# Kernel optimization log

Hardware: AMD Instinct MI355X
Metric: run time of the kernel (lower is better)

Reference implementation:

```python
import jax, jax.numpy as jnp
import numpy as np

H = 1024          # hidden_size
NH = 16           # num_attention_heads
HD = H // NH      # attention_head_size (= rotary_dim)
I = 4096          # intermediate_size
E = 8             # num_experts
TOPK = 2          # top_k_experts
EPS = 1e-12       # layer_norm_eps
B, S = 2, 2048


def setup_inputs() -> dict:
    key = jax.random.key(0)
    ks = jax.random.split(key, 12)
    sc = 0.02
    return {
        "hidden_states": jax.random.normal(ks[0], (B, S, H), dtype=jnp.float32),
        "Wq": jax.random.normal(ks[1], (H, H), dtype=jnp.float32) * sc,
        "Wk": jax.random.normal(ks[2], (H, H), dtype=jnp.float32) * sc,
        "Wv": jax.random.normal(ks[3], (H, H), dtype=jnp.float32) * sc,
        "Wd": jax.random.normal(ks[4], (H, H), dtype=jnp.float32) * sc,
        "bd": jnp.zeros((H,), dtype=jnp.float32),
        "ln1_g": jnp.ones((H,), dtype=jnp.float32),
        "ln1_b": jnp.zeros((H,), dtype=jnp.float32),
        "Wg": jax.random.normal(ks[5], (H, E), dtype=jnp.float32) * sc,
        "W1": jax.random.normal(ks[6], (E, H, I), dtype=jnp.float32) * sc,
        "W2": jax.random.normal(ks[7], (E, I, H), dtype=jnp.float32) * sc,
        "ln2_g": jnp.ones((H,), dtype=jnp.float32),
        "ln2_b": jnp.zeros((H,), dtype=jnp.float32),
    }


def _layernorm(x, g, b):
    mu = jnp.mean(x, axis=-1, keepdims=True)
    var = jnp.mean(jnp.square(x - mu), axis=-1, keepdims=True)
    return (x - mu) * jax.lax.rsqrt(var + EPS) * g + b


def _rotate_half(x):
    x1, x2 = x[..., : HD // 2], x[..., HD // 2 :]
    return jnp.concatenate((-x2, x1), axis=-1)


def _rope_cos_sin(seq_len, dtype):
    inv_freq = 1.0 / (10000.0 ** (jnp.arange(0, HD, 2, dtype=jnp.float32) / HD))
    t = jnp.arange(seq_len, dtype=jnp.float32)
    freqs = jnp.einsum("i,j->ij", t, inv_freq)          # [S, HD/2]
    emb = jnp.concatenate((freqs, freqs), axis=-1)        # [S, HD]
    return jnp.cos(emb).astype(dtype)[None, None], jnp.sin(emb).astype(dtype)[None, None]


def reference(hidden_states, Wq, Wk, Wv, Wd, bd, ln1_g, ln1_b, Wg, W1, W2, ln2_g, ln2_b):
    b, s, h = hidden_states.shape
    x = hidden_states

    # ---- multi-head attention with RoPE ----
    def heads(z):  # [B,S,H] -> [B,NH,S,HD]
        return z.reshape(b, s, NH, HD).transpose(0, 2, 1, 3)

    q = heads(x @ Wq)
    k = heads(x @ Wk)
    v = heads(x @ Wv)
    cos, sin = _rope_cos_sin(s, q.dtype)
    q = q * cos + _rotate_half(q) * sin
    k = k * cos + _rotate_half(k) * sin

    scores = jnp.einsum("bnqd,bnkd->bnqk", q, k) / jnp.sqrt(jnp.float32(HD)).astype(q.dtype)
    probs = jax.nn.softmax(scores, axis=-1)
    ctx = jnp.einsum("bnqk,bnkd->bnqd", probs, v)
    ctx = ctx.transpose(0, 2, 1, 3).reshape(b, s, h)

    attn_out = ctx @ Wd + bd
    hs = _layernorm(attn_out + x, ln1_g, ln1_b)  # residual + LN

    # ---- MoE ----
    T = b * s
    xt = hs.reshape(T, h)
    router_logits = xt @ Wg                                   # [T, E]
    probs_r = jax.nn.softmax(router_logits.astype(jnp.float32), axis=-1)
    rw, sel = jax.lax.top_k(probs_r, TOPK)                    # [T, K]
    rw = rw / jnp.sum(rw, axis=-1, keepdims=True)

    # aux load-balancing loss
    f_i = jnp.sum(jax.nn.one_hot(sel, E, dtype=jnp.float32), axis=(0, 1)) / T
    P_i = jnp.mean(probs_r, axis=0)
    aux_loss = E * jnp.sum(f_i * P_i)

    # per-token combine weights [T, E] (0 for unrouted experts)
    combine = jnp.zeros((T, E), dtype=jnp.float32)
    combine = combine.at[jnp.arange(T)[:, None], sel].add(rw)
    combine = combine.astype(xt.dtype)

    moe_out = jnp.zeros_like(xt)
    for e in range(E):  # small fixed expert loop
        ye = jax.nn.gelu(xt @ W1[e], approximate=False) @ W2[e]
        moe_out = moe_out + combine[:, e : e + 1] * ye
    moe_out = moe_out.reshape(b, s, h)

    out = _layernorm(hs + moe_out, ln2_g, ln2_b)
    return out, aux_loss
```

## Files before the change

### kernel.cpp

```cpp
#include <hip/hip_runtime.h>
#include <hip/hip_bf16.h>
#include <math.h>

#define H_ 1024
#define NH_ 16
#define HD_ 64
#define I_ 4096
#define E_ 8
#define B_ 2
#define S_ 2048
#define T_ 4096

#define MAXSLOTS 9216
#define MAXTILES 72

typedef __attribute__((ext_vector_type(8))) short short8v;
typedef __attribute__((ext_vector_type(4))) float f32x4;

#define GLOAD16(g, l) __builtin_amdgcn_global_load_lds((const __attribute__((address_space(1))) void*)(g), (__attribute__((address_space(3))) void*)(l), 16, 0, 0)

static __device__ inline unsigned short f2bf(float x) {
    __hip_bfloat16 h = __float2bfloat16(x);
    unsigned short u;
    __builtin_memcpy(&u, &h, 2);
    return u;
}
static __device__ inline float bf2f(unsigned short u) {
    __hip_bfloat16 h;
    __builtin_memcpy(&h, &u, 2);
    return __bfloat162float(h);
}

static __device__ inline float gelu_fast(float x) {
    float z  = x * 0.70710678118654752f;
    float az = fabsf(z);
    float t  = __builtin_amdgcn_rcpf(fmaf(0.3275911f, az, 1.f));
    float p  = fmaf(1.061405429f, t, -1.453152027f);
    p = fmaf(p, t, 1.421413741f);
    p = fmaf(p, t, -0.284496736f);
    p = fmaf(p, t, 0.254829592f);
    p = p * t;
    float e = __expf(-az*az);
    float er = 1.f - p*e;
    er = (z < 0.f) ? -er : er;
    return 0.5f * x * (1.f + er);
}

__global__ __launch_bounds__(256) void prep_inputs(
    const float* __restrict__ x,
    const float* __restrict__ Wq, const float* __restrict__ Wk,
    const float* __restrict__ Wv, const float* __restrict__ Wd,
    __hip_bfloat16* __restrict__ xa_hi, __hip_bfloat16* __restrict__ xa_lo,
    __hip_bfloat16* __restrict__ wqkv_h, __hip_bfloat16* __restrict__ wqkv_l,
    __hip_bfloat16* __restrict__ wd_h, __hip_bfloat16* __restrict__ wd_l)
{
    __shared__ float t[64][65];
    const int bid = blockIdx.x;
    const int tid = threadIdx.x;
    if (bid < 4096) {
        int i = bid * 256 + tid;
        float4 v = ((const float4*)x)[i];
        unsigned short h0 = f2bf(v.x), h1 = f2bf(v.y), h2 = f2bf(v.z), h3 = f2bf(v.w);
        unsigned short l0 = f2bf(v.x - bf2f(h0)), l1 = f2bf(v.y - bf2f(h1));
        unsigned short l2 = f2bf(v.z - bf2f(h2)), l3 = f2bf(v.w - bf2f(h3));
        uint2 ph = make_uint2((unsigned)h0 | ((unsigned)h1 << 16), (unsigned)h2 | ((unsigned)h3 << 16));
        uint2 pl = make_uint2((unsigned)l0 | ((unsigned)l1 << 16), (unsigned)l2 | ((unsigned)l3 << 16));
        *(uint2*)((char*)xa_hi + (size_t)i*8) = ph;
        *(uint2*)((char*)xa_lo + (size_t)i*8) = pl;
        return;
    }
    int tt = bid - 4096;
    int bx = tt & 15, by = (tt >> 4) & 15, z = tt >> 8;
    const float* in = (z==0) ? Wq : (z==1) ? Wk : (z==2) ? Wv : Wd;
    __hip_bfloat16* oh = (z<3) ? (wqkv_h + (size_t)z*1024*1024) : wd_h;
    __hip_bfloat16* ol = (z<3) ? (wqkv_l + (size_t)z*1024*1024) : wd_l;
    int k0 = by*64, n0 = bx*64;
    #pragma unroll
    for (int it=0; it<4; ++it) {
        int lin = it*256 + tid;
        int r = lin >> 4, c4 = (lin & 15) << 2;
        float4 v = *(const float4*)&in[(size_t)(k0+r)*1024 + n0 + c4];
        t[r][c4] = v.x; t[r][c4+1] = v.y; t[r][c4+2] = v.z; t[r][c4+3] = v.w;
    }
    __syncthreads();
    #pragma unroll
    for (int it=0; it<4; ++it) {
        int lin = it*256 + tid;
        int r = lin >> 4, c4 = (lin & 15) << 2;
        float v0 = t[c4][r], v1 = t[c4+1][r], v2 = t[c4+2][r], v3 = t[c4+3][r];
        ushort4 hh, ll;
        hh.x = f2bf(v0); hh.y = f2bf(v1); hh.z = f2bf(v2); hh.w = f2bf(v3);
        ll.x = f2bf(v0 - bf2f(hh.x)); ll.y = f2bf(v1 - bf2f(hh.y));
        ll.z = f2bf(v2 - bf2f(hh.z)); ll.w = f2bf(v3 - bf2f(hh.w));
        size_t o = (size_t)(n0+r)*1024 + k0 + c4;
        *(ushort4*)&oh[o] = hh;
        *(ushort4*)&ol[o] = ll;
    }
}

__global__ __launch_bounds__(256) void transpose_bf16(
    const float* __restrict__ in, __hip_bfloat16* __restrict__ outp, int K, int N)
{
    __shared__ float t[64][65];
    size_t eoff = (size_t)blockIdx.z * (size_t)K * (size_t)N;
    int k0 = blockIdx.y*64, n0 = blockIdx.x*64;
    int tid = threadIdx.x;
    #pragma unroll
    for (int it=0; it<4; ++it) {
        int lin = it*256 + tid;
        int r = lin >> 4, c4 = (lin & 15) << 2;
        float4 v = *(const float4*)&in[eoff + (size_t)(k0+r)*N + n0 + c4];
        t[r][c4] = v.x; t[r][c4+1] = v.y; t[r][c4+2] = v.z; t[r][c4+3] = v.w;
    }
    __syncthreads();
    #pragma unroll
    for (int it=0; it<4; ++it) {
        int lin = it*256 + tid;
        int r = lin >> 4, c4 = (lin & 15) << 2;
        ushort4 o;
        o.x = f2bf(t[c4][r]);   o.y = f2bf(t[c4+1][r]);
        o.z = f2bf(t[c4+2][r]); o.w = f2bf(t[c4+3][r]);
        *(ushort4*)&outp[eoff + (size_t)(n0+r)*K + k0 + c4] = o;
    }
}

__global__ __launch_bounds__(256, 2) void wd_gemm_zero(
    const __hip_bfloat16* __restrict__ Ah, const __hip_bfloat16* __restrict__ Al,
    const __hip_bfloat16* __restrict__ Bh, const __hip_bfloat16* __restrict__ Bl,
    float* __restrict__ C, const float* __restrict__ bias,
    float* __restrict__ moe_out, float* __restrict__ misc16)
{
    const int bid = blockIdx.x;
    const int tid = threadIdx.x;
    if (bid >= 256) {
        int z = bid - 256;
        ((float4*)moe_out)[z*256 + tid] = (float4){0.f,0.f,0.f,0.f};
        if (z == 0 && tid < 16) misc16[tid] = 0.f;
        return;
    }
    const int N = 1024, K = 1024;
    const int w = tid >> 6, lane = tid & 63;
    const int xcd = bid & 7, ix = bid >> 3;
    const int by = xcd*4 + ix / 8;
    const int bx = ix % 8;

    __shared__ __align__(16) char smem[65536];
    const int AH = 0, AL = 16384, BH = 32768, BL = 49152;

    const int laneg = lane >> 3;
    const int k2sw = ((lane & 7) ^ laneg) << 4;
    const int l15 = lane & 15, l4 = lane >> 4;
    const int wr = w >> 1, wc = w & 1;

    f32x4 acc[4][4];
    #pragma unroll
    for (int m=0;m<4;m++)
        #pragma unroll
        for (int n=0;n<4;n++) acc[m][n] = (f32x4){0.f,0.f,0.f,0.f};

    for (int k0 = 0; k0 < K; k0 += 64) {
        __syncthreads();
        #pragma unroll
        for (int qq=0;qq<4;qq++) {
            int arow = by*128 + (w*4+qq)*8 + laneg;
            int brow = bx*128 + (w*4+qq)*8 + laneg;
            size_t aoff = ((size_t)arow*K + k0)*2 + k2sw;
            size_t boff = ((size_t)brow*K + k0)*2 + k2sw;
            GLOAD16((const char*)Ah + aoff, smem + AH + (w*4+qq)*1024);
            GLOAD16((const char*)Al + aoff, smem + AL + (w*4+qq)*1024);
            GLOAD16((const char*)Bh + boff, smem + BH + (w*4+qq)*1024);
            GLOAD16((const char*)Bl + boff, smem + BL + (w*4+qq)*1024);
        }
        __syncthreads();

        short8v ahf[4][2], alf[4][2], bhf[4][2], blf[4][2];
        #pragma unroll
        for (int m=0;m<4;m++) {
            int row = wr*64 + m*16 + l15;
            int rb = row << 7, rsw = (row & 7) << 4;
            #pragma unroll
            for (int s=0;s<2;s++) {
                int off = rb + ((s*64 + (l4<<4)) ^ rsw);
                ahf[m][s] = *(const short8v*)(smem + AH + off);
                alf[m][s] = *(const short8v*)(smem + AL + off);
            }
        }
        #pragma unroll
        for (int n=0;n<4;n++) {
            int row = wc*64 + n*16 + l15;
            int rb = row << 7, rsw = (row & 7) << 4;
            #pragma unroll
            for (int s=0;s<2;s++) {
                int off = rb + ((s*64 + (l4<<4)) ^ rsw);
                bhf[n][s] = *(const short8v*)(smem + BH + off);
                blf[n][s] = *(const short8v*)(smem + BL + off);
            }
        }
        #pragma unroll
        for (int m=0;m<4;m++)
            #pragma unroll
            for (int n=0;n<4;n++)
                #pragma unroll
                for (int s=0;s<2;s++) {
                    acc[m][n] = __builtin_amdgcn_mfma_f32_16x16x32_bf16(ahf[m][s], bhf[n][s], acc[m][n], 0, 0, 0);
                    acc[m][n] = __builtin_amdgcn_mfma_f32_16x16x32_bf16(ahf[m][s], blf[n][s], acc[m][n], 0, 0, 0);
                    acc[m][n] = __builtin_amdgcn_mfma_f32_16x16x32_bf16(alf[m][s], bhf[n][s], acc[m][n], 0, 0, 0);
                }
    }

    #pragma unroll
    for (int m=0;m<4;m++)
        #pragma unroll
        for (int j=0;j<4;j++) {
            int orow = by*128 + wr*64 + m*16 + l4*4 + j;
            #pragma unroll
            for (int n=0;n<4;n++) {
                int ocol = bx*128 + wc*64 + n*16 + l15;
                C[(size_t)orow*N + ocol] = acc[m][n][j] + bias[ocol];
            }
        }
}

__global__ __launch_bounds__(256, 2) void fused_qkv_w12(
    const __hip_bfloat16* __restrict__ Ah, const __hip_bfloat16* __restrict__ Al,
    const __hip_bfloat16* __restrict__ Bh, const __hip_bfloat16* __restrict__ Bl,
    float* __restrict__ C,
    const float* __restrict__ W1, const float* __restrict__ W2,
    __hip_bfloat16* __restrict__ W1t, __hip_bfloat16* __restrict__ W2t)
{
    __shared__ __align__(16) char smem[65536];
    const int tid = threadIdx.x;
    const int bid = blockIdx.x;

    if (bid < 768) {
        const int N = 3072, K = 1024;
        const int w = tid >> 6, lane = tid & 63;
        const int xcd = bid & 7, ix = bid >> 3;
        const int by = xcd*4 + ix / 24;
        const int bx = ix % 24;
        const int AH = 0, AL = 16384, BH = 32768, BL = 49152;
        const int laneg = lane >> 3;
        const int k2sw = ((lane & 7) ^ laneg) << 4;
        const int l15 = lane & 15, l4 = lane >> 4;
        const int wr = w >> 1, wc = w & 1;

        f32x4 acc[4][4];
        #pragma unroll
        for (int m=0;m<4;m++)
            #pragma unroll
            for (int n=0;n<4;n++) acc[m][n] = (f32x4){0.f,0.f,0.f,0.f};

        for (int k0 = 0; k0 < K; k0 += 64) {
            __syncthreads();
            #pragma unroll
            for (int qq=0;qq<4;qq++) {
                int arow = by*128 + (w*4+qq)*8 + laneg;
                int brow = bx*128 + (w*4+qq)*8 + laneg;
                size_t aoff = ((size_t)arow*K + k0)*2 + k2sw;
                size_t boff = ((size_t)brow*K + k0)*2 + k2sw;
                GLOAD16((const char*)Ah + aoff, smem + AH + (w*4+qq)*1024);
                GLOAD16((const char*)Al + aoff, smem + AL + (w*4+qq)*1024);
                GLOAD16((const char*)Bh + boff, smem + BH + (w*4+qq)*1024);
                GLOAD16((const char*)Bl + boff, smem + BL + (w*4+qq)*1024);
            }
            __syncthreads();

            short8v ahf[4][2], alf[4][2], bhf[4][2], blf[4][2];
            #pragma unroll
            for (int m=0;m<4;m++) {
                int row = wr*64 + m*16 + l15;
                int rb = row << 7, rsw = (row & 7) << 4;
                #pragma unroll
                for (int s=0;s<2;s++) {
                    int off = rb + ((s*64 + (l4<<4)) ^ rsw);
                    ahf[m][s] = *(const short8v*)(smem + AH + off);
                    alf[m][s] = *(const short8v*)(smem + AL + off);
                }
            }
            #pragma unroll
            for (int n=0;n<4;n++) {
                int row = wc*64 + n*16 + l15;
                int rb = row << 7, rsw = (row & 7) << 4;
                #pragma unroll
                for (int s=0;s<2;s++) {
                    int off = rb + ((s*64 + (l4<<4)) ^ rsw);
                    bhf[n][s] = *(const short8v*)(smem + BH + off);
                    blf[n][s] = *(const short8v*)(smem + BL + off);
                }
            }
            #pragma unroll
            for (int m=0;m<4;m++)
                #pragma unroll
                for (int n=0;n<4;n++)
                    #pragma unroll
                    for (int s=0;s<2;s++) {
                        acc[m][n] = __builtin_amdgcn_mfma_f32_16x16x32_bf16(ahf[m][s], bhf[n][s], acc[m][n], 0, 0, 0);
                        acc[m][n] = __builtin_amdgcn_mfma_f32_16x16x32_bf16(ahf[m][s], blf[n][s], acc[m][n], 0, 0, 0);
                        acc[m][n] = __builtin_amdgcn_mfma_f32_16x16x32_bf16(alf[m][s], bhf[n][s], acc[m][n], 0, 0, 0);
                    }
        }

        #pragma unroll
        for (int m=0;m<4;m++)
            #pragma unroll
            for (int j=0;j<4;j++) {
                int orow = by*128 + wr*64 + m*16 + l4*4 + j;
                #pragma unroll
                for (int n=0;n<4;n++) {
                    int ocol = bx*128 + wc*64 + n*16 + l15;
                    C[(size_t)orow*N + ocol] = acc[m][n][j];
                }
            }
        return;
    }

    int t = bid - 768;
    const float* src;
    __hip_bfloat16* dst;
    int K, N;
    if (t < 8192) { src = W1; dst = W1t; K = 1024; N = 4096; }
    else          { t -= 8192; src = W2; dst = W2t; K = 4096; N = 1024; }
    const int nb_n = N >> 6;
    int bx = t % nb_n;
    int rest = t / nb_n;
    int by = rest % (K >> 6);
    int bz = rest / (K >> 6);
    size_t eoff = (size_t)bz * (size_t)K * (size_t)N;
    int k0 = by*64, n0 = bx*64;
    float (*tt)[65] = (float(*)[65])smem;
    #pragma unroll
    for (int it=0; it<4; ++it) {
        int lin = it*256 + tid;
        int r = lin >> 4, c4 = (lin & 15) << 2;
        float4 v = *(const float4*)&src[eoff + (size_t)(k0+r)*N + n0 + c4];
        tt[r][c4] = v.x; tt[r][c4+1] = v.y; tt[r][c4+2] = v.z; tt[r][c4+3] = v.w;
    }
    __syncthreads();
    #pragma unroll
    for (int it=0; it<4; ++it) {
        int lin = it*256 + tid;
        int r = lin >> 4, c4 = (lin & 15) << 2;
        ushort4 o;
        o.x = f2bf(tt[c4][r]);   o.y = f2bf(tt[c4+1][r]);
        o.z = f2bf(tt[c4+2][r]); o.w = f2bf(tt[c4+3][r]);
        *(ushort4*)&dst[eoff + (size_t)(n0+r)*K + k0 + c4] = o;
    }
}

template<int MODE, bool PE>
__global__ __launch_bounds__(256) void moe_mfma(
    const __hip_bfloat16* __restrict__ A,
    const __hip_bfloat16* __restrict__ Bt,
    __hip_bfloat16* __restrict__ y1,
    float* __restrict__ moe_out,
    const int* __restrict__ slot_token,
    const float* __restrict__ slot_w,
    const int* __restrict__ tile_expert,
    const int* __restrict__ cnt_ptr,
    const int* __restrict__ base_ptr,
    int N, int K, int nbx)
{
    const int tid = threadIdx.x;
    const int w = tid >> 6, lane = tid & 63;

    int bx, slot0, y1row0;
    const __hip_bfloat16* Bp;
    if (PE) {
        bx = blockIdx.x;
        int tloc = blockIdx.y;
        if ((tloc << 7) >= *cnt_ptr) return;
        slot0 = *base_ptr + (tloc << 7);
        y1row0 = tloc << 7;
        Bp = Bt;
    } else {
        const int wg = blockIdx.x;
        const int xcd = wg & 7, ix = wg >> 3;
        const int byc = (int)(gridDim.x >> 3) / nbx;
        int gt = xcd*byc + ix % byc;
        bx = ix / byc;
        if (gt >= *cnt_ptr) return;
        int e = tile_expert[gt];
        Bp = Bt + (size_t)e * (size_t)K * (size_t)N;
        slot0 = gt << 7;
        y1row0 = gt << 7;
    }

    __shared__ __align__(16) char smem[32768];

    const int laneg = lane >> 3;
    const int k2sw = ((lane & 7) ^ laneg) << 4;

    int tokq[4];
    if (MODE == 2) {
        #pragma unroll
        for (int qq=0;qq<4;qq++) {
            int t0 = slot_token[slot0 + (w*4+qq)*8 + laneg];
            tokq[qq] = t0 < 0 ? 0 : t0;
        }
    }

    f32x4 acc[4][4];
    #pragma unroll
    for (int m=0;m<4;m++)
        #pragma unroll
        for (int n=0;n<4;n++) acc[m][n] = (f32x4){0.f,0.f,0.f,0.f};

    const int l15 = lane & 15;
    const int l4  = lane >> 4;
    const int wr = w >> 1, wc = w & 1;

    for (int k0 = 0; k0 < K; k0 += 64) {
        __syncthreads();
        #pragma unroll
        for (int qq=0;qq<4;qq++) {
            const char* ga;
            if (MODE == 2) {
                ga = (const char*)A + (((size_t)tokq[qq])*K + k0)*2 + k2sw;
            } else {
                int row = y1row0 + (w*4+qq)*8 + laneg;
                ga = (const char*)A + ((size_t)row*K + k0)*2 + k2sw;
            }
            GLOAD16(ga, smem + (w*4+qq)*1024);
        }
        #pragma unroll
        for (int qq=0;qq<4;qq++) {
            int row = bx*128 + (w*4+qq)*8 + laneg;
            const char* gb = (const char*)Bp + ((size_t)row*K + k0)*2 + k2sw;
            GLOAD16(gb, smem + 16384 + (w*4+qq)*1024);
        }
        __syncthreads();

        short8v a_frag[4][2], b_frag[4][2];
        #pragma unroll
        for (int m=0;m<4;m++) {
            int row = wr*64 + m*16 + l15;
            int rb = row << 7;
            #pragma unroll
            for (int s=0;s<2;s++) {
                int off = rb + ((s*64 + (l4<<4)) ^ ((row&7)<<4));
                a_frag[m][s] = *(const short8v*)(smem + off);
            }
        }
        #pragma unroll
        for (int n=0;n<4;n++) {
            int row = wc*64 + n*16 + l15;
            int rb = row << 7;
            #pragma unroll
            for (int s=0;s<2;s++) {
                int off = rb + ((s*64 + (l4<<4)) ^ ((row&7)<<4));
                b_frag[n][s] = *(const short8v*)(smem + 16384 + off);
            }
        }
        #pragma unroll
        for (int m=0;m<4;m++)
            #pragma unroll
            for (int n=0;n<4;n++) {
                acc[m][n] = __builtin_amdgcn_mfma_f32_16x16x32_bf16(a_frag[m][0], b_frag[n][0], acc[m][n], 0, 0, 0);
                acc[m][n] = __builtin_amdgcn_mfma_f32_16x16x32_bf16(a_frag[m][1], b_frag[n][1], acc[m][n], 0, 0, 0);
            }
    }

    if (MODE == 3) {
        #pragma unroll
        for (int m=0;m<4;m++) {
            #pragma unroll
            for (int j=0;j<4;j++) {
                int orow = wr*64 + m*16 + l4*4 + j;
                int slot = slot0 + orow;
                int tok = slot_token[slot];
                if (tok < 0) continue;
                float sw = slot_w[slot];
                #pragma unroll
                for (int n=0;n<4;n++) {
                    int ocol = bx*128 + wc*64 + n*16 + l15;
                    atomicAdd(&moe_out[(size_t)tok*H_ + ocol], sw * acc[m][n][j]);
                }
            }
        }
    } else {
        __syncthreads();
        #pragma unroll
        for (int m=0;m<4;m++)
            #pragma unroll
            for (int j=0;j<4;j++) {
                int orow = wr*64 + m*16 + l4*4 + j;
                #pragma unroll
                for (int n=0;n<4;n++) {
                    int ocol = wc*64 + n*16 + l15;
                    unsigned short g = f2bf(gelu_fast(acc[m][n][j]));
                    *(unsigned short*)(smem + orow*256 + ocol*2) = g;
                }
            }
        __syncthreads();
        #pragma unroll
        for (int s=0;s<8;s++) {
            int row = w*32 + s*4 + l4;
            short8v v = *(const short8v*)(smem + row*256 + l15*16);
            *(short8v*)((char*)y1 + ((size_t)(y1row0 + row)*N + bx*128 + l15*8)*2) = v;
        }
    }
}

__global__ __launch_bounds__(256) void rope_vsplit(
    const float* __restrict__ qkv,
    __hip_bfloat16* __restrict__ qh, __hip_bfloat16* __restrict__ ql,
    __hip_bfloat16* __restrict__ kh, __hip_bfloat16* __restrict__ kl,
    __hip_bfloat16* __restrict__ vth, __hip_bfloat16* __restrict__ vtl)
{
    __shared__ float t[64][65];
    const int bid = blockIdx.x;
    const int tid = threadIdx.x;
    if (bid < 8192) {
        int idx = bid * 256 + tid;
        int i = idx & 31;
        int n = (idx >> 5) & (NH_-1);
        int tk = idx >> 9;
        int b = tk >> 11;
        int pos = tk & (S_ - 1);
        float inv = exp2f((float)i * (-13.287712379549449f / 32.f));
        float ang = (float)pos * inv;
        float c = cosf(ang), s = sinf(ang);
        size_t base = (size_t)tk*3072 + (size_t)n*64;
        size_t obase = ((size_t)(b*NH_ + n)*S_ + pos)*64;

        float q1 = qkv[base+i], q2 = qkv[base+i+32];
        float qo1 = (q1*c - q2*s)*0.125f;
        float qo2 = (q2*c + q1*s)*0.125f;
        unsigned short h1 = f2bf(qo1), h2 = f2bf(qo2);
        qh[obase+i]    = *(__hip_bfloat16*)&h1;
        qh[obase+i+32] = *(__hip_bfloat16*)&h2;
        unsigned short lo1 = f2bf(qo1 - bf2f(h1)), lo2 = f2bf(qo2 - bf2f(h2));
        ql[obase+i]    = *(__hip_bfloat16*)&lo1;
        ql[obase+i+32] = *(__hip_bfloat16*)&lo2;

        float k1 = qkv[base+1024+i], k2 = qkv[base+1024+i+32];
        float ko1 = k1*c - k2*s;
        float ko2 = k2*c + k1*s;
        unsigned short kh1 = f2bf(ko1), kh2 = f2bf(ko2);
        kh[obase+i]    = *(__hip_bfloat16*)&kh1;
        kh[obase+i+32] = *(__hip_bfloat16*)&kh2;
        unsigned short kl1 = f2bf(ko1 - bf2f(kh1)), kl2 = f2bf(ko2 - bf2f(kh2));
        kl[obase+i]    = *(__hip_bfloat16*)&kl1;
        kl[obase+i+32] = *(__hip_bfloat16*)&kl2;
        return;
    }
    int tt = bid - 8192;
    const int s0 = (tt & 31)*64;
    const int hn = (tt >> 5) & 15;
    const int b  = tt >> 9;
    #pragma unroll
    for (int it=0; it<4; ++it) {
        int lin = it*256 + tid;
        int r = lin >> 4, c4 = (lin & 15) << 2;
        float4 vv = *(const float4*)&qkv[(size_t)(b*S_ + s0 + r)*3072 + 2048 + hn*64 + c4];
        t[r][c4] = vv.x; t[r][c4+1] = vv.y; t[r][c4+2] = vv.z; t[r][c4+3] = vv.w;
    }
    __syncthreads();
    size_t obase = (size_t)(b*NH_ + hn)*64*S_;
    #pragma unroll
    for (int it=0; it<4; ++it) {
        int lin = it*256 + tid;
        int d = lin >> 4, c4 = (lin & 15) << 2;
        float v0 = t[c4][d], v1 = t[c4+1][d], v2 = t[c4+2][d], v3 = t[c4+3][d];
        ushort4 hh, ll;
        hh.x = f2bf(v0); hh.y = f2bf(v1); hh.z = f2bf(v2); hh.w = f2bf(v3);
        ll.x = f2bf(v0 - bf2f(hh.x)); ll.y = f2bf(v1 - bf2f(hh.y));
        ll.z = f2bf(v2 - bf2f(hh.z)); ll.w = f2bf(v3 - bf2f(hh.w));
        size_t o = obase + (size_t)d*S_ + s0 + c4;
        *(ushort4*)&vth[o] = hh;
        *(ushort4*)&vtl[o] = ll;
    }
}

__global__ __launch_bounds__(256) void attn_mfma(
    const __hip_bfloat16* __restrict__ qh, const __hip_bfloat16* __restrict__ ql,
    const __hip_bfloat16* __restrict__ kh, const __hip_bfloat16* __restrict__ kl,
    const __hip_bfloat16* __restrict__ vth, const __hip_bfloat16* __restrict__ vtl,
    __hip_bfloat16* __restrict__ ctx_hi, __hip_bfloat16* __restrict__ ctx_lo)
{
    const int wg = blockIdx.x;
    const int xcd = wg & 7;
    const int ix = wg >> 3;
    const int head = xcd*4 + (ix >> 4);
    const int qt = ix & 15;
    const int b = head >> 4, hn = head & 15;

    const int tid = threadIdx.x;
    const int w = tid >> 6, lane = tid & 63;
    const int l15 = lane & 15, l4 = lane >> 4;
    const int laneg = lane >> 3;
    const int k2sw = ((lane & 7) ^ laneg) << 4;

    __shared__ __align__(16) char smem[32768];
    const int KHo = 0, KLo = 8192, VHo = 16384, VLo = 24576;
    const int PHo = 0, PLo = 8192;

    const size_t kbase = (size_t)head*S_*64;
    const size_t vbase = (size_t)head*64*S_;

    short8v qhf[2][2], qlf[2][2];
    #pragma unroll
    for (int m=0;m<2;m++) {
        #pragma unroll
        for (int qq=0;qq<2;qq++) {
            int c = w*2 + qq;
            int row = qt*128 + m*64 + c*8 + laneg;
            size_t off = (kbase + (size_t)row*64)*2 + k2sw;
            GLOAD16((const char*)qh + off, smem + KHo + c*1024);
            GLOAD16((const char*)ql + off, smem + KLo + c*1024);
        }
        __syncthreads();
        {
            int row = w*16 + l15;
            int rsw = (row & 7) << 4;
            #pragma unroll
            for (int s=0;s<2;s++) {
                int off = row*128 + ((s*64 + l4*16) ^ rsw);
                qhf[m][s] = *(const short8v*)(smem + KHo + off);
                qlf[m][s] = *(const short8v*)(smem + KLo + off);
            }
        }
        __syncthreads();
    }

    f32x4 acc[2][4];
    #pragma unroll
    for (int m=0;m<2;m++)
        #pragma unroll
        for (int db=0;db<4;db++) acc[m][db] = (f32x4){0.f,0.f,0.f,0.f};
    float lrun[2][4] = {{0.f,0.f,0.f,0.f},{0.f,0.f,0.f,0.f}};

    for (int kt=0; kt<S_/64; ++kt) {
        #pragma unroll
        for (int qq=0;qq<2;qq++) {
            int c = w*2 + qq;
            int r8 = c*8 + laneg;
            size_t koff = (kbase + (size_t)(kt*64 + r8)*64)*2 + k2sw;
            GLOAD16((const char*)kh + koff, smem + KHo + c*1024);
            GLOAD16((const char*)kl + koff, smem + KLo + c*1024);
            size_t voff = (vbase + (size_t)r8*S_ + kt*64)*2 + k2sw;
            GLOAD16((const char*)vth + voff, smem + VHo + c*1024);
            GLOAD16((const char*)vtl + voff, smem + VLo + c*1024);
        }
        __syncthreads();

        f32x4 s_acc[2][4];
        #pragma unroll
        for (int cb=0;cb<4;cb++) {
            s_acc[0][cb] = (f32x4){0.f,0.f,0.f,0.f};
            s_acc[1][cb] = (f32x4){0.f,0.f,0.f,0.f};
            int row = cb*16 + l15;
            int rsw = (row & 7) << 4;
            #pragma unroll
            for (int s=0;s<2;s++) {
                int off = row*128 + ((s*64 + l4*16) ^ rsw);
                short8v khf = *(const short8v*)(smem + KHo + off);
                short8v klf = *(const short8v*)(smem + KLo + off);
                s_acc[0][cb] = __builtin_amdgcn_mfma_f32_16x16x32_bf16(qhf[0][s], khf, s_acc[0][cb], 0, 0, 0);
                s_acc[0][cb] = __builtin_amdgcn_mfma_f32_16x16x32_bf16(qhf[0][s], klf, s_acc[0][cb], 0, 0, 0);
                s_acc[0][cb] = __builtin_amdgcn_mfma_f32_16x16x32_bf16(qlf[0][s], khf, s_acc[0][cb], 0, 0, 0);
                s_acc[1][cb] = __builtin_amdgcn_mfma_f32_16x16x32_bf16(qhf[1][s], khf, s_acc[1][cb], 0, 0, 0);
                s_acc[1][cb] = __builtin_amdgcn_mfma_f32_16x16x32_bf16(qhf[1][s], klf, s_acc[1][cb], 0, 0, 0);
                s_acc[1][cb] = __builtin_amdgcn_mfma_f32_16x16x32_bf16(qlf[1][s], khf, s_acc[1][cb], 0, 0, 0);
            }
        }
        __syncthreads();

        #pragma unroll
        for (int m=0;m<2;m++) {
            #pragma unroll
            for (int cb=0;cb<4;cb++)
                #pragma unroll
                for (int j=0;j<4;j++) {
                    float p = __expf(s_acc[m][cb][j]);
                    lrun[m][j] += p;
                    int prow = w*16 + l4*4 + j;
                    unsigned short hh = f2bf(p);
                    unsigned short ll = f2bf(p - bf2f(hh));
                    int off = prow*128 + (((cb*16 + l15)*2) ^ ((prow&7)<<4));
                    *(unsigned short*)(smem + PHo + off) = hh;
                    *(unsigned short*)(smem + PLo + off) = ll;
                }
            asm volatile("s_waitcnt lgkmcnt(0)" ::: "memory");
            __builtin_amdgcn_sched_barrier(0);

            short8v pah[2], pal[2];
            {
                int row = w*16 + l15;
                int rsw = (row & 7) << 4;
                #pragma unroll
                for (int s=0;s<2;s++) {
                    int off = row*128 + ((s*64 + l4*16) ^ rsw);
                    pah[s] = *(const short8v*)(smem + PHo + off);
                    pal[s] = *(const short8v*)(smem + PLo + off);
                }
            }
            #pragma unroll
            for (int db=0;db<4;db++) {
                int row = db*16 + l15;
                int rsw = (row & 7) << 4;
                #pragma unroll
                for (int s=0;s<2;s++) {
                    int off = row*128 + ((s*64 + l4*16) ^ rsw);
                    short8v vhf = *(const short8v*)(smem + VHo + off);
                    short8v vlf = *(const short8v*)(smem + VLo + off);
                    acc[m][db] = __builtin_amdgcn_mfma_f32_16x16x32_bf16(pah[s], vhf, acc[m][db], 0, 0, 0);
                    acc[m][db] = __builtin_amdgcn_mfma_f32_16x16x32_bf16(pah[s], vlf, acc[m][db], 0, 0, 0);
                    acc[m][db] = __builtin_amdgcn_mfma_f32_16x16x32_bf16(pal[s], vhf, acc[m][db], 0, 0, 0);
                }
            }
            __builtin_amdgcn_sched_barrier(0);
        }
        __syncthreads();
    }

    #pragma unroll
    for (int m=0;m<2;m++) {
        #pragma unroll
        for (int j=0;j<4;j++) {
            float s = lrun[m][j];
            #pragma unroll
            for (int mk=8;mk;mk>>=1) s += __shfl_xor(s, mk);
            lrun[m][j] = s;
        }
        #pragma unroll
        for (int db=0;db<4;db++)
            #pragma unroll
            for (int j=0;j<4;j++) {
                int qrow = qt*128 + m*64 + w*16 + l4*4 + j;
                float o = acc[m][db][j] / lrun[m][j];
                unsigned short hh = f2bf(o);
                unsigned short ll = f2bf(o - bf2f(hh));
                size_t oidx = (size_t)(b*S_ + qrow)*H_ + hn*64 + db*16 + l15;
                ctx_hi[oidx] = *(__hip_bfloat16*)&hh;
                ctx_lo[oidx] = *(__hip_bfloat16*)&ll;
            }
    }
}

__global__ __launch_bounds__(256) void ln_kernel(
    const float* __restrict__ a, const float* __restrict__ res,
    const float* __restrict__ g, const float* __restrict__ beta,
    float* __restrict__ out, __hip_bfloat16* __restrict__ outb)
{
    int row = blockIdx.x, tid = threadIdx.x;
    const float4 va = ((const float4*)(a + (size_t)row*H_))[tid];
    const float4 vr = ((const float4*)(res + (size_t)row*H_))[tid];
    float x0=va.x+vr.x, x1=va.y+vr.y, x2=va.z+vr.z, x3=va.w+vr.w;
    float s  = x0+x1+x2+x3;
    float ss = x0*x0 + x1*x1 + x2*x2 + x3*x3;
    #pragma unroll
    for (int off=32; off; off>>=1) { s += __shfl_xor(s, off); ss += __shfl_xor(ss, off); }
    __shared__ float red[8];
    if ((tid&63)==0) { red[tid>>6]=s; red[4+(tid>>6)]=ss; }
    __syncthreads();
    if (tid==0) { red[0]=red[0]+red[1]+red[2]+red[3]; red[4]=red[4]+red[5]+red[6]+red[7]; }
    __syncthreads();
    float mu  = red[0] * (1.f/H_);
    float var = red[4] * (1.f/H_) - mu*mu;
    float rs = rsqrtf(fmaxf(var, 0.f) + 1e-12f);
    const float4 vg = ((const float4*)g)[tid];
    const float4 vb = ((const float4*)beta)[tid];
    float4 vo;
    vo.x = (x0-mu)*rs*vg.x + vb.x;
    vo.y = (x1-mu)*rs*vg.y + vb.y;
    vo.z = (x2-mu)*rs*vg.z + vb.z;
    vo.w = (x3-mu)*rs*vg.w + vb.w;
    ((float4*)(out + (size_t)row*H_))[tid] = vo;
    if (outb) {
        unsigned int p0 = (unsigned)f2bf(vo.x) | ((unsigned)f2bf(vo.y) << 16);
        unsigned int p1 = (unsigned)f2bf(vo.z) | ((unsigned)f2bf(vo.w) << 16);
        ((uint2*)(outb + (size_t)row*H_))[tid] = make_uint2(p0, p1);
    }
}

__global__ __launch_bounds__(256) void router_kernel(
    const float* __restrict__ hs, const float* __restrict__ Wg,
    int* __restrict__ tok_e, float* __restrict__ tok_w,
    int* __restrict__ counts, float* __restrict__ P_sum)
{
    const int w = threadIdx.x >> 6, lane = threadIdx.x & 63;
    float psum[E_];
    int cnt[E_];
    #pragma unroll
    for (int e=0;e<E_;e++){ psum[e]=0.f; cnt[e]=0; }

    for (int it=0; it<16; ++it) {
        int t = blockIdx.x*64 + it*4 + w;
        const float* row = hs + (size_t)t * H_;
        float acc[E_];
        #pragma unroll
        for (int e=0;e<E_;e++) acc[e]=0.f;
        for (int i16=0; i16<16; ++i16) {
            int i = i16*64 + lane;
            float xv = row[i];
            const float* wg = Wg + (size_t)i*E_;
            #pragma unroll
            for (int e=0;e<E_;e++) acc[e] = fmaf(xv, wg[e], acc[e]);
        }
        #pragma unroll
        for (int e=0;e<E_;e++) {
            float vv = acc[e];
            #pragma unroll
            for (int off=32; off; off>>=1) vv += __shfl_xor(vv, off);
            acc[e] = vv;
        }
        float mx = acc[0];
        #pragma unroll
        for (int e=1;e<E_;e++) mx = fmaxf(mx, acc[e]);
        float p[E_], se=0.f;
        #pragma unroll
        for (int e=0;e<E_;e++){ p[e] = __expf(acc[e]-mx); se += p[e]; }
        float isv = 1.f/se;
        #pragma unroll
        for (int e=0;e<E_;e++){ p[e]*=isv; psum[e] += p[e]; }
        int e1=0;
        #pragma unroll
        for (int e=1;e<E_;e++) if (p[e] > p[e1]) e1=e;
        int e2 = (e1==0)?1:0;
        #pragma unroll
        for (int e=0;e<E_;e++) if (e!=e1 && p[e] > p[e2]) e2=e;
        #pragma unroll
        for (int e=0;e<E_;e++) cnt[e] += (e==e1?1:0) + (e==e2?1:0);
        if (lane==0) {
            float w1=p[e1], w2=p[e2], si=1.f/(w1+w2);
            tok_e[t*2]=e1; tok_e[t*2+1]=e2;
            tok_w[t*2]=w1*si; tok_w[t*2+1]=w2*si;
        }
    }
    if (lane==0) {
        #pragma unroll
        for (int e=0;e<E_;e++) {
            atomicAdd(&P_sum[e], psum[e]);
            atomicAdd(&counts[e], cnt[e]);
        }
    }
}

__global__ void router_finalize(
    const int* __restrict__ counts, const float* __restrict__ P_sum,
    int* __restrict__ base, int* __restrict__ cursor,
    int* __restrict__ cnt_pad, int* __restrict__ ntiles,
    int* __restrict__ slot_token, int* __restrict__ tile_expert,
    float* __restrict__ aux_out)
{
    __shared__ int sbase[E_+1];
    if (threadIdx.x == 0) {
        int bacc = 0;
        float aux = 0.f;
        for (int e=0;e<E_;e++) {
            sbase[e] = bacc; base[e] = bacc;
            int cp = (counts[e] + 127) & ~127;
            cnt_pad[e] = cp;
            bacc += cp;
            cursor[e] = 0;
            aux += ((float)counts[e]/(float)T_) * (P_sum[e]/(float)T_);
        }
        sbase[E_] = bacc;
        *ntiles = bacc >> 7;
        *aux_out = (float)E_ * aux;
    }
    __syncthreads();
    for (int sIdx = (int)threadIdx.x; sIdx < MAXSLOTS; sIdx += (int)blockDim.x)
        slot_token[sIdx] = -1;
    for (int tt = (int)threadIdx.x; tt < MAXTILES; tt += (int)blockDim.x) {
        int s = tt*128;
        int e = E_-1;
        for (int qe=0; qe<E_; ++qe) if (s < sbase[qe+1]) { e = qe; break; }
        tile_expert[tt] = e;
    }
}

__global__ void scatter_slots(
    const int* __restrict__ tok_e, const float* __restrict__ tok_w,
    const int* __restrict__ base, int* __restrict__ cursor,
    int* __restrict__ slot_token, float* __restrict__ slot_w)
{
    int t = blockIdx.x*blockDim.x + threadIdx.x;
    if (t >= T_) return;
    #pragma unroll
    for (int j=0;j<2;j++) {
        int e = tok_e[t*2+j];
        int pos = atomicAdd(&cursor[e], 1);
        int s = base[e] + pos;
        slot_token[s] = t;
        slot_w[s] = tok_w[t*2+j];
    }
}

extern "C" void kernel_launch(void* const* d_in, const int* in_sizes, int n_in,
                              void* d_out, int out_size, void* d_ws, size_t ws_size,
                              hipStream_t stream)
{
    const float* x    = (const float*)d_in[0];
    const float* Wq   = (const float*)d_in[1];
    const float* Wk   = (const float*)d_in[2];
    const float* Wv   = (const float*)d_in[3];
    const float* Wd   = (const float*)d_in[4];
    const float* bd   = (const float*)d_in[5];
    const float* ln1g = (const float*)d_in[6];
    const float* ln1b = (const float*)d_in[7];
    const float* Wg   = (const float*)d_in[8];
    const float* W1   = (const float*)d_in[9];
    const float* W2   = (const float*)d_in[10];
    const float* ln2g = (const float*)d_in[11];
    const float* ln2b = (const float*)d_in[12];
    float* out = (float*)d_out;

    float* f0 = (float*)d_ws;
    const size_t M1 = 1u << 20;
    float* qkv      = f0;
    float* attn_out = f0 + 12*M1;
    float* hs       = f0;
    float* moe_out  = f0 + 4*M1;
    __hip_bfloat16* hs_b = (__hip_bfloat16*)(f0 + 16*M1);

    float* misc = f0 + 18*M1;
    int*   misc_i = (int*)misc;
    int*   tok_e   = misc_i;
    float* tok_w   = misc + 8192;
    int*   slot_tok= misc_i + 16384;
    float* slot_w  = misc + 25600;
    int*   counts  = misc_i + 34816;
    float* P_sum   = misc + 34824;
    int*   cursor  = misc_i + 34832;
    int*   basep   = misc_i + 34840;
    int*   cnt_pad = misc_i + 34848;
    int*   ntiles  = misc_i + 34856;
    int*   tile_ex = misc_i + 34857;

    float* off_p = f0 + 18*M1 + 65536;
    __hip_bfloat16* xa_hi = (__hip_bfloat16*)(off_p);
    __hip_bfloat16* xa_lo = (__hip_bfloat16*)(off_p + 2*M1);
    __hip_bfloat16* at_qh = (__hip_bfloat16*)(off_p + 4*M1);
    __hip_bfloat16* at_ql = (__hip_bfloat16*)(off_p + 6*M1);
    __hip_bfloat16* at_kh = (__hip_bfloat16*)(off_p + 8*M1);
    __hip_bfloat16* at_kl = (__hip_bfloat16*)(off_p + 10*M1);
    __hip_bfloat16* at_vh = (__hip_bfloat16*)(off_p + 12*M1);
    __hip_bfloat16* at_vl = (__hip_bfloat16*)(off_p + 14*M1);
    __hip_bfloat16* wqkv_h = (__hip_bfloat16*)(off_p + 16*M1);
    __hip_bfloat16* wqkv_l = (__hip_bfloat16*)(off_p + 16*M1 + 3*(M1/2));
    __hip_bfloat16* wd_h = (__hip_bfloat16*)(off_p + 19*M1);
    __hip_bfloat16* wd_l = (__hip_bfloat16*)(off_p + 19*M1 + M1/2);

    const bool FULL = ws_size >= (size_t)300*1024*1024;
    __hip_bfloat16* W1t = (__hip_bfloat16*)(off_p + 20*M1);
    __hip_bfloat16* W2t = (__hip_bfloat16*)(off_p + 36*M1);
    __hip_bfloat16* y1F = (__hip_bfloat16*)(off_p);
    float* wreg = off_p + 4*M1;

    dim3 blk(256);

    prep_inputs<<<dim3(5120), blk, 0, stream>>>(x, Wq, Wk, Wv, Wd, xa_hi, xa_lo, wqkv_h, wqkv_l, wd_h, wd_l);

    if (FULL) {
        fused_qkv_w12<<<dim3(768 + 8192 + 8192), blk, 0, stream>>>(
            xa_hi, xa_lo, wqkv_h, wqkv_l, qkv, W1, W2, W1t, W2t);
    } else {
        fused_qkv_w12<<<dim3(768), blk, 0, stream>>>(
            xa_hi, xa_lo, wqkv_h, wqkv_l, qkv, nullptr, nullptr, nullptr, nullptr);
    }

    rope_vsplit<<<dim3(8192 + 1024), blk, 0, stream>>>(qkv, at_qh, at_ql, at_kh, at_kl, at_vh, at_vl);

    attn_mfma<<<dim3(B_*NH_*(S_/128)), blk, 0, stream>>>(at_qh, at_ql, at_kh, at_kl, at_vh, at_vl, xa_hi, xa_lo);

    wd_gemm_zero<<<dim3(256 + 4096), blk, 0, stream>>>(xa_hi, xa_lo, wd_h, wd_l, attn_out, bd, moe_out, misc + 34816);

    ln_kernel<<<T_, blk, 0, stream>>>(attn_out, x, ln1g, ln1b, hs, hs_b);

    router_kernel<<<T_/64, blk, 0, stream>>>(hs, Wg, tok_e, tok_w, counts, P_sum);
    router_finalize<<<1, blk, 0, stream>>>(counts, P_sum, basep, cursor, cnt_pad, ntiles,
                                           slot_tok, tile_ex, out + (size_t)T_*H_);
    scatter_slots<<<T_/256, blk, 0, stream>>>(tok_e, tok_w, basep, cursor, slot_tok, slot_w);

    if (FULL) {
        moe_mfma<2,false><<<dim3(MAXTILES*32), blk, 0, stream>>>(
            hs_b, W1t, y1F, nullptr, slot_tok, slot_w, tile_ex, ntiles, nullptr, I_, H_, 32);
        moe_mfma<3,false><<<dim3(MAXTILES*8), blk, 0, stream>>>(
            y1F, W2t, nullptr, moe_out, slot_tok, slot_w, tile_ex, ntiles, nullptr, H_, I_, 8);
    } else {
        __hip_bfloat16* w1t = (__hip_bfloat16*)wreg;
        __hip_bfloat16* w2t = (__hip_bfloat16*)(wreg + 2*M1);
        __hip_bfloat16* y1  = (__hip_bfloat16*)(wreg + 4*M1);
        for (int e=0; e<E_; ++e) {
            transpose_bf16<<<dim3(I_/64, H_/64, 1), blk, 0, stream>>>(W1 + (size_t)e*H_*I_, w1t, H_, I_);
            moe_mfma<2,true><<<dim3(I_/128, 32), blk, 0, stream>>>(
                hs_b, w1t, y1, nullptr, slot_tok, slot_w, nullptr, cnt_pad+e, basep+e, I_, H_, 0);
            transpose_bf16<<<dim3(H_/64, I_/64, 1), blk, 0, stream>>>(W2 + (size_t)e*I_*H_, w2t, I_, H_);
            moe_mfma<3,true><<<dim3(H_/128, 32), blk, 0, stream>>>(
                y1, w2t, nullptr, moe_out, slot_tok, slot_w, nullptr, cnt_pad+e, basep+e, H_, I_, 0);
        }
    }

    ln_kernel<<<T_, blk, 0, stream>>>(moe_out, hs, ln2g, ln2b, out, nullptr);
}
```

Baseline: 751.6 us.

## Fuse router logits and top-2 selection into first layernorm kernel

The router GEMV, softmax and top-2 selection now run inside the first layernorm kernel, one block per token, reusing the normalized values already held in registers. This removes a separate router launch and its re-read of hs. Per-token probabilities go to a buffer, and the single-block finalize kernel reduces counts and probability sums itself instead of relying on global atomics. The cost is that one block now serially scans 4096 tokens in finalize, and the layernorm kernel gains an extra barrier.

Measured after the change: 693.3 us. -7.8%, faster.

```diff
diff --git a/kernel.cpp b/kernel.cpp
--- a/kernel.cpp
+++ b/kernel.cpp
@@ -738,10 +738,13 @@
     }
 }
 
+template<bool ROUTER>
 __global__ __launch_bounds__(256) void ln_kernel(
     const float* __restrict__ a, const float* __restrict__ res,
     const float* __restrict__ g, const float* __restrict__ beta,
-    float* __restrict__ out, __hip_bfloat16* __restrict__ outb)
+    float* __restrict__ out, __hip_bfloat16* __restrict__ outb,
+    const float* __restrict__ Wg, int* __restrict__ tok_e,
+    float* __restrict__ tok_w, float* __restrict__ P_part)
 {
     int row = blockIdx.x, tid = threadIdx.x;
     const float4 va = ((const float4*)(a + (size_t)row*H_))[tid];
@@ -772,98 +775,125 @@
         unsigned int p1 = (unsigned)f2bf(vo.z) | ((unsigned)f2bf(vo.w) << 16);
         ((uint2*)(outb + (size_t)row*H_))[tid] = make_uint2(p0, p1);
     }
-}
-
-__global__ __launch_bounds__(256) void router_kernel(
-    const float* __restrict__ hs, const float* __restrict__ Wg,
-    int* __restrict__ tok_e, float* __restrict__ tok_w,
-    int* __restrict__ counts, float* __restrict__ P_sum)
-{
-    const int w = threadIdx.x >> 6, lane = threadIdx.x & 63;
-    float psum[E_];
-    int cnt[E_];
-    #pragma unroll
-    for (int e=0;e<E_;e++){ psum[e]=0.f; cnt[e]=0; }
-
-    for (int it=0; it<16; ++it) {
-        int t = blockIdx.x*64 + it*4 + w;
-        const float* row = hs + (size_t)t * H_;
-        float acc[E_];
-        #pragma unroll
-        for (int e=0;e<E_;e++) acc[e]=0.f;
-        for (int i16=0; i16<16; ++i16) {
-            int i = i16*64 + lane;
-            float xv = row[i];
-            const float* wg = Wg + (size_t)i*E_;
-            #pragma unroll
-            for (int e=0;e<E_;e++) acc[e] = fmaf(xv, wg[e], acc[e]);
+    if (ROUTER) {
+        float xs0 = vo.x, xs1 = vo.y, xs2 = vo.z, xs3 = vo.w;
+        const float4* wg4 = (const float4*)(Wg + (size_t)(tid*4)*E_);
+        float pl[E_];
+        #pragma unroll
+        for (int e=0;e<E_;e++) pl[e] = 0.f;
+        #pragma unroll
+        for (int r=0;r<4;r++) {
+            float xv = (r==0)?xs0:(r==1)?xs1:(r==2)?xs2:xs3;
+            float4 wa = wg4[r*2], wb = wg4[r*2+1];
+            pl[0] = fmaf(xv, wa.x, pl[0]);
+            pl[1] = fmaf(xv, wa.y, pl[1]);
+            pl[2] = fmaf(xv, wa.z, pl[2]);
+            pl[3] = fmaf(xv, wa.w, pl[3]);
+            pl[4] = fmaf(xv, wb.x, pl[4]);
+            pl[5] = fmaf(xv, wb.y, pl[5]);
+            pl[6] = fmaf(xv, wb.z, pl[6]);
+            pl[7] = fmaf(xv, wb.w, pl[7]);
         }
         #pragma unroll
         for (int e=0;e<E_;e++) {
-            float vv = acc[e];
-            #pragma unroll
-            for (int off=32; off; off>>=1) vv += __shfl_xor(vv, off);
-            acc[e] = vv;
-        }
-        float mx = acc[0];
-        #pragma unroll
-        for (int e=1;e<E_;e++) mx = fmaxf(mx, acc[e]);
-        float p[E_], se=0.f;
-        #pragma unroll
-        for (int e=0;e<E_;e++){ p[e] = __expf(acc[e]-mx); se += p[e]; }
-        float isv = 1.f/se;
-        #pragma unroll
-        for (int e=0;e<E_;e++){ p[e]*=isv; psum[e] += p[e]; }
-        int e1=0;
-        #pragma unroll
-        for (int e=1;e<E_;e++) if (p[e] > p[e1]) e1=e;
-        int e2 = (e1==0)?1:0;
-        #pragma unroll
-        for (int e=0;e<E_;e++) if (e!=e1 && p[e] > p[e2]) e2=e;
-        #pragma unroll
-        for (int e=0;e<E_;e++) cnt[e] += (e==e1?1:0) + (e==e2?1:0);
-        if (lane==0) {
+            float v = pl[e];
+            #pragma unroll
+            for (int off=32; off; off>>=1) v += __shfl_xor(v, off);
+            pl[e] = v;
+        }
+        __shared__ float rr[4][E_];
+        if ((tid&63)==0) {
+            #pragma unroll
+            for (int e=0;e<E_;e++) rr[tid>>6][e] = pl[e];
+        }
+        __syncthreads();
+        if (tid == 0) {
+            float lg[E_];
+            #pragma unroll
+            for (int e=0;e<E_;e++) lg[e] = rr[0][e]+rr[1][e]+rr[2][e]+rr[3][e];
+            float mx = lg[0];
+            #pragma unroll
+            for (int e=1;e<E_;e++) mx = fmaxf(mx, lg[e]);
+            float p[E_], se=0.f;
+            #pragma unroll
+            for (int e=0;e<E_;e++){ p[e] = __expf(lg[e]-mx); se += p[e]; }
+            float isv = 1.f/se;
+            #pragma unroll
+            for (int e=0;e<E_;e++) p[e] *= isv;
+            int e1=0;
+            #pragma unroll
+            for (int e=1;e<E_;e++) if (p[e] > p[e1]) e1=e;
+            int e2 = (e1==0)?1:0;
+            #pragma unroll
+            for (int e=0;e<E_;e++) if (e!=e1 && p[e] > p[e2]) e2=e;
             float w1=p[e1], w2=p[e2], si=1.f/(w1+w2);
-            tok_e[t*2]=e1; tok_e[t*2+1]=e2;
-            tok_w[t*2]=w1*si; tok_w[t*2+1]=w2*si;
-        }
-    }
-    if (lane==0) {
-        #pragma unroll
-        for (int e=0;e<E_;e++) {
-            atomicAdd(&P_sum[e], psum[e]);
-            atomicAdd(&counts[e], cnt[e]);
+            tok_e[row*2]=e1; tok_e[row*2+1]=e2;
+            tok_w[row*2]=w1*si; tok_w[row*2+1]=w2*si;
+            float4 pa, pb;
+            pa.x=p[0]; pa.y=p[1]; pa.z=p[2]; pa.w=p[3];
+            pb.x=p[4]; pb.y=p[5]; pb.z=p[6]; pb.w=p[7];
+            ((float4*)&P_part[(size_t)row*E_])[0] = pa;
+            ((float4*)&P_part[(size_t)row*E_])[1] = pb;
         }
     }
 }
 
 __global__ void router_finalize(
-    const int* __restrict__ counts, const float* __restrict__ P_sum,
+    const int* __restrict__ tok_e, const float* __restrict__ P_part,
     int* __restrict__ base, int* __restrict__ cursor,
     int* __restrict__ cnt_pad, int* __restrict__ ntiles,
     int* __restrict__ slot_token, int* __restrict__ tile_expert,
     float* __restrict__ aux_out)
 {
+    __shared__ int scnt[E_];
+    __shared__ float sps[E_];
     __shared__ int sbase[E_+1];
-    if (threadIdx.x == 0) {
+    const int tid = threadIdx.x;
+    if (tid < E_) { scnt[tid] = 0; sps[tid] = 0.f; }
+    __syncthreads();
+
+    int cnt[E_];
+    float ps[E_];
+    #pragma unroll
+    for (int e=0;e<E_;e++){ cnt[e]=0; ps[e]=0.f; }
+    for (int t = tid; t < T_; t += 256) {
+        int e1 = tok_e[t*2], e2 = tok_e[t*2+1];
+        #pragma unroll
+        for (int e=0;e<E_;e++) cnt[e] += (e==e1 ? 1 : 0) + (e==e2 ? 1 : 0);
+        float4 a = ((const float4*)&P_part[(size_t)t*E_])[0];
+        float4 b = ((const float4*)&P_part[(size_t)t*E_])[1];
+        ps[0]+=a.x; ps[1]+=a.y; ps[2]+=a.z; ps[3]+=a.w;
+        ps[4]+=b.x; ps[5]+=b.y; ps[6]+=b.z; ps[7]+=b.w;
+    }
+    #pragma unroll
+    for (int e=0;e<E_;e++) {
+        int c = cnt[e];
+        float v = ps[e];
+        #pragma unroll
+        for (int off=32; off; off>>=1) { c += __shfl_xor(c, off); v += __shfl_xor(v, off); }
+        if ((tid&63)==0) { atomicAdd(&scnt[e], c); atomicAdd(&sps[e], v); }
+    }
+    __syncthreads();
+
+    if (tid == 0) {
         int bacc = 0;
         float aux = 0.f;
         for (int e=0;e<E_;e++) {
             sbase[e] = bacc; base[e] = bacc;
-            int cp = (counts[e] + 127) & ~127;
+            int cp = (scnt[e] + 127) & ~127;
             cnt_pad[e] = cp;
             bacc += cp;
             cursor[e] = 0;
-            aux += ((float)counts[e]/(float)T_) * (P_sum[e]/(float)T_);
+            aux += ((float)scnt[e]/(float)T_) * (sps[e]/(float)T_);
         }
         sbase[E_] = bacc;
         *ntiles = bacc >> 7;
         *aux_out = (float)E_ * aux;
     }
     __syncthreads();
-    for (int sIdx = (int)threadIdx.x; sIdx < MAXSLOTS; sIdx += (int)blockDim.x)
+    for (int sIdx = tid; sIdx < MAXSLOTS; sIdx += (int)blockDim.x)
         slot_token[sIdx] = -1;
-    for (int tt = (int)threadIdx.x; tt < MAXTILES; tt += (int)blockDim.x) {
+    for (int tt = tid; tt < MAXTILES; tt += (int)blockDim.x) {
         int s = tt*128;
         int e = E_-1;
         for (int qe=0; qe<E_; ++qe) if (s < sbase[qe+1]) { e = qe; break; }
@@ -913,6 +943,7 @@
     float* attn_out = f0 + 12*M1;
     float* hs       = f0;
     float* moe_out  = f0 + 4*M1;
+    float* P_part   = f0 + 8*M1;
     __hip_bfloat16* hs_b = (__hip_bfloat16*)(f0 + 16*M1);
 
     float* misc = f0 + 18*M1;
@@ -921,8 +952,6 @@
     float* tok_w   = misc + 8192;
     int*   slot_tok= misc_i + 16384;
     float* slot_w  = misc + 25600;
-    int*   counts  = misc_i + 34816;
-    float* P_sum   = misc + 34824;
     int*   cursor  = misc_i + 34832;
     int*   basep   = misc_i + 34840;
     int*   cnt_pad = misc_i + 34848;
@@ -967,10 +996,10 @@
 
     wd_gemm_zero<<<dim3(256 + 4096), blk, 0, stream>>>(xa_hi, xa_lo, wd_h, wd_l, attn_out, bd, moe_out, misc + 34816);
 
-    ln_kernel<<<T_, blk, 0, stream>>>(attn_out, x, ln1g, ln1b, hs, hs_b);
-
-    router_kernel<<<T_/64, blk, 0, stream>>>(hs, Wg, tok_e, tok_w, counts, P_sum);
-    router_finalize<<<1, blk, 0, stream>>>(counts, P_sum, basep, cursor, cnt_pad, ntiles,
+    ln_kernel<true><<<T_, blk, 0, stream>>>(attn_out, x, ln1g, ln1b, hs, hs_b,
+                                            Wg, tok_e, tok_w, P_part);
+
+    router_finalize<<<1, blk, 0, stream>>>(tok_e, P_part, basep, cursor, cnt_pad, ntiles,
                                            slot_tok, tile_ex, out + (size_t)T_*H_);
     scatter_slots<<<T_/256, blk, 0, stream>>>(tok_e, tok_w, basep, cursor, slot_tok, slot_w);
 
@@ -993,5 +1022,6 @@
         }
     }
 
-    ln_kernel<<<T_, blk, 0, stream>>>(moe_out, hs, ln2g, ln2b, out, nullptr);
-}
+    ln_kernel<false><<<T_, blk, 0, stream>>>(moe_out, hs, ln2g, ln2b, out, nullptr,
+                                             nullptr, nullptr, nullptr, nullptr);
+}
```
